# Optimization experiments

Measured on AMD Instinct MI355X. Metric: run time of the kernel, lower is better.

The kernel has to match this reference:

```python
import jax, jax.numpy as jnp
import numpy as np

S, B, H2, M = 4096, 16, 1024, 4096  # seq_len, batch, 2*hidden_size, max_number_of_entries


def setup_inputs() -> dict:
    key = jax.random.key(0)
    ks = jax.random.split(key, 5)
    return {
        "encoder_outputs": jax.random.normal(ks[0], (S, B, H2), jnp.float32),
        "state": jax.random.normal(ks[1], (B, H2), jnp.float32),
        "previous_attention": jax.random.uniform(ks[2], (B, M), jnp.float32),
        "attn_w": jax.random.normal(ks[3], (H2, H2), jnp.float32) / np.sqrt(H2).astype(np.float32),
        "attn_b": jnp.zeros((H2,), jnp.float32),
        "time_w": jax.random.normal(ks[4], (M, M), jnp.float32) / np.sqrt(M).astype(np.float32),
        "time_b": jnp.zeros((M,), jnp.float32),
    }


def reference(encoder_outputs, state, previous_attention, attn_w, attn_b, time_w, time_b):
    # encoder_outputs: [S, B, 2H]; state: [B, 2H]; previous_attention: [B, M]
    seq_len = encoder_outputs.shape[0]
    # attend(): Linear on state, then per-timestep dot product with encoder output.
    # The original Python loop over S timesteps + torch.cat is one batched matvec:
    altered_state = state @ attn_w.T + attn_b                      # [B, 2H]
    weights = jnp.einsum('bd,sbd->bs', altered_state, encoder_outputs)  # [B, S]
    # time_attention branch (its result is computed but unused by the outputs,
    # mirrored here for faithfulness to the original forward)
    apw = previous_attention @ time_w.T + time_b                   # [B, M]
    prev_probs = jax.nn.softmax(apw[:, :seq_len], axis=0)          # softmax over batch dim, as in original
    _adjusted_weights = prev_probs * weights                       # dead value in the original module
    # final softmax attention + weighted sum over encoder outputs
    normalized_weights = jax.nn.softmax(weights, axis=1)           # [B, S]
    attention_applied = jnp.einsum('bs,sbd->bd', normalized_weights, encoder_outputs)  # [B, 2H]
    return attention_applied, normalized_weights
```

## Files before the change

kernel.cpp:

```cpp
#include <hip/hip_runtime.h>
#include <cstdint>
#include <cstddef>

#define S_LEN 4096
#define B_SZ 16
#define H2D 1024
#define P_PER_B 128

__device__ __forceinline__ float dot4(float4 a, float4 b) {
    return a.x * b.x + a.y * b.y + a.z * b.z + a.w * b.w;
}
__device__ __forceinline__ void axpy4(float4& acc, float w, float4 v) {
    acc.x += w * v.x; acc.y += w * v.y; acc.z += w * v.z; acc.w += w * v.w;
}

__global__ __launch_bounds__(256) void k_altered(const float* __restrict__ state,
                                                 const float* __restrict__ attn_w,
                                                 const float* __restrict__ attn_b,
                                                 float* __restrict__ altered) {
    const int i = (blockIdx.x * 256 + threadIdx.x) >> 6;
    const int lane = threadIdx.x & 63;
    const float4* w4 = (const float4*)(attn_w + (size_t)i * H2D);
    float4 r[4];
#pragma unroll
    for (int j = 0; j < 4; ++j) r[j] = w4[lane + 64 * j];
    const float bias = attn_b[i];
    for (int b = 0; b < B_SZ; ++b) {
        const float4* s4 = (const float4*)(state + b * H2D);
        float p = 0.f;
#pragma unroll
        for (int j = 0; j < 4; ++j) p += dot4(r[j], s4[lane + 64 * j]);
#pragma unroll
        for (int off = 32; off; off >>= 1) p += __shfl_xor(p, off, 64);
        if (lane == 0) altered[b * H2D + i] = p + bias;
    }
}

__global__ __launch_bounds__(256) void k_flash(const float* __restrict__ enc,
                                               const float* __restrict__ altered,
                                               float* __restrict__ w_raw,
                                               float* __restrict__ pm,
                                               float* __restrict__ pl,
                                               float* __restrict__ pacc) {
    const int b = blockIdx.y;
    const int wave = threadIdx.x >> 6, lane = threadIdx.x & 63;
    const int slot = blockIdx.x * 4 + wave;

    const float4* a4 = (const float4*)(altered + b * H2D);
    float4 af[4];
#pragma unroll
    for (int j = 0; j < 4; ++j) af[j] = a4[lane + 64 * j];

    float m = -1e30f, l = 0.f;
    float4 acc[4];
#pragma unroll
    for (int j = 0; j < 4; ++j) acc[j] = make_float4(0.f, 0.f, 0.f, 0.f);

    const int s0 = slot * 32;
    for (int k = 0; k < 32; k += 4) {
        float4 e[4][4];
        float p[4];
#pragma unroll
        for (int r = 0; r < 4; ++r) {
            const float4* e4 = (const float4*)(enc + ((size_t)(s0 + k + r) * B_SZ + b) * H2D);
#pragma unroll
            for (int j = 0; j < 4; ++j) e[r][j] = e4[lane + 64 * j];
        }
#pragma unroll
        for (int r = 0; r < 4; ++r) {
            p[r] = 0.f;
#pragma unroll
            for (int j = 0; j < 4; ++j) p[r] += dot4(af[j], e[r][j]);
        }
#pragma unroll
        for (int off = 32; off; off >>= 1)
#pragma unroll
            for (int r = 0; r < 4; ++r) p[r] += __shfl_xor(p[r], off, 64);
        if (lane == 0) {
#pragma unroll
            for (int r = 0; r < 4; ++r) w_raw[b * S_LEN + s0 + k + r] = p[r];
        }
        float mn = m;
#pragma unroll
        for (int r = 0; r < 4; ++r) mn = fmaxf(mn, p[r]);
        const float sc = __expf(m - mn);
        float ex[4];
#pragma unroll
        for (int r = 0; r < 4; ++r) ex[r] = __expf(p[r] - mn);
        l = l * sc + ex[0] + ex[1] + ex[2] + ex[3];
#pragma unroll
        for (int j = 0; j < 4; ++j) {
            acc[j].x *= sc; acc[j].y *= sc; acc[j].z *= sc; acc[j].w *= sc;
#pragma unroll
            for (int r = 0; r < 4; ++r) axpy4(acc[j], ex[r], e[r][j]);
        }
        m = mn;
    }

    const size_t pi = (size_t)(b * P_PER_B + slot);
    if (lane == 0) { pm[pi] = m; pl[pi] = l; }
    float4* o = (float4*)(pacc + pi * H2D);
#pragma unroll
    for (int j = 0; j < 4; ++j) o[lane + 64 * j] = acc[j];
}

__global__ __launch_bounds__(256) void k_fin1(const float* __restrict__ pm,
                                              const float* __restrict__ pl,
                                              const float* __restrict__ w_raw,
                                              float* __restrict__ cexp,
                                              float* __restrict__ MZ,
                                              float* __restrict__ out_attn,
                                              float* __restrict__ out_nw) {
    const int b = blockIdx.x, t = threadIdx.x;
    const int wave = t >> 6, lane = t & 63;
    __shared__ float sw[4];
    const float mv = (t < P_PER_B) ? pm[b * P_PER_B + t] : -1e30f;
    float mm = mv;
#pragma unroll
    for (int off = 32; off; off >>= 1) mm = fmaxf(mm, __shfl_xor(mm, off, 64));
    if (lane == 0) sw[wave] = mm;
    __syncthreads();
    const float M = fmaxf(fmaxf(sw[0], sw[1]), fmaxf(sw[2], sw[3]));
    const float e = (t < P_PER_B) ? __expf(mv - M) : 0.f;
    float zl = (t < P_PER_B) ? e * pl[b * P_PER_B + t] : 0.f;
#pragma unroll
    for (int off = 32; off; off >>= 1) zl += __shfl_xor(zl, off, 64);
    __syncthreads();
    if (lane == 0) sw[wave] = zl;
    __syncthreads();
    const float invZ = 1.f / (sw[0] + sw[1] + sw[2] + sw[3]);
    if (t < P_PER_B) cexp[b * P_PER_B + t] = e;
    if (t == 0) { MZ[2 * b] = M; MZ[2 * b + 1] = invZ; }
    ((float4*)(out_attn + b * H2D))[t] = make_float4(0.f, 0.f, 0.f, 0.f);
    const float4* wr = (const float4*)(w_raw + b * S_LEN);
    float4* on = (float4*)(out_nw + b * S_LEN);
#pragma unroll
    for (int i = 0; i < 4; ++i) {
        const int idx = t + 256 * i;
        const float4 v = wr[idx];
        on[idx] = make_float4(__expf(v.x - M) * invZ, __expf(v.y - M) * invZ,
                              __expf(v.z - M) * invZ, __expf(v.w - M) * invZ);
    }
}

__global__ __launch_bounds__(256) void k_fin2(const float* __restrict__ pacc,
                                              const float* __restrict__ cexp,
                                              const float* __restrict__ MZ,
                                              float* __restrict__ out_attn) {
    const int b = blockIdx.x, pg = blockIdx.y, t = threadIdx.x;
    const float invZ = MZ[2 * b + 1];
    const float* cb = cexp + b * P_PER_B + pg * 64;
    const float4* base = (const float4*)(pacc + (size_t)(b * P_PER_B + pg * 64) * H2D);
    float4 s = make_float4(0.f, 0.f, 0.f, 0.f);
#pragma unroll 8
    for (int p = 0; p < 64; ++p) {
        const float c = cb[p];
        axpy4(s, c, base[(size_t)p * 256 + t]);
    }
    float* o = out_attn + b * H2D + 4 * t;
    atomicAdd(o + 0, s.x * invZ);
    atomicAdd(o + 1, s.y * invZ);
    atomicAdd(o + 2, s.z * invZ);
    atomicAdd(o + 3, s.w * invZ);
}

extern "C" void kernel_launch(void* const* d_in, const int* in_sizes, int n_in,
                              void* d_out, int out_size, void* d_ws, size_t ws_size,
                              hipStream_t stream) {
    const float* enc    = (const float*)d_in[0];
    const float* state  = (const float*)d_in[1];
    const float* attn_w = (const float*)d_in[3];
    const float* attn_b = (const float*)d_in[4];

    float* ws = (float*)d_ws;
    float* altered = ws;
    float* w_raw   = altered + 16384;
    float* pm      = w_raw + 65536;
    float* pl      = pm + 2048;
    float* cexp    = pl + 2048;
    float* MZ      = cexp + 2048;
    float* pacc    = MZ + 1024;

    float* out_attn = (float*)d_out;
    float* out_nw   = (float*)d_out + B_SZ * H2D;

    hipLaunchKernelGGL(k_altered, dim3(256), dim3(256), 0, stream,
                       state, attn_w, attn_b, altered);
    hipLaunchKernelGGL(k_flash, dim3(32, B_SZ), dim3(256), 0, stream,
                       enc, altered, w_raw, pm, pl, pacc);
    hipLaunchKernelGGL(k_fin1, dim3(B_SZ), dim3(256), 0, stream,
                       pm, pl, w_raw, cexp, MZ, out_attn, out_nw);
    hipLaunchKernelGGL(k_fin2, dim3(B_SZ, 2), dim3(256), 0, stream,
                       pacc, cexp, MZ, out_attn);
}
```

Baseline: 409.0 us.

## Double flash-attention blocks and merge wave partials in shared memory

Each k_flash wave now handles 16 sequence rows instead of 32, and the grid has twice as many blocks. This is meant to raise occupancy and memory-level parallelism on the latency-bound encoder stream. The four waves of a block merge their online-softmax partials (max, sum, accumulator) through LDS, so each block writes one partial. That halves the partials per batch and the pacc traffic read by k_fin2. The cost is an extra __syncthreads plus LDS staging per block, and an occupancy hint in launch_bounds that may constrain register allocation.

```diff
diff --git a/kernel.cpp b/kernel.cpp
--- a/kernel.cpp
+++ b/kernel.cpp
@@ -5,7 +5,7 @@
 #define S_LEN 4096
 #define B_SZ 16
 #define H2D 1024
-#define P_PER_B 128
+#define P_PER_B 64
 
 __device__ __forceinline__ float dot4(float4 a, float4 b) {
     return a.x * b.x + a.y * b.y + a.z * b.z + a.w * b.w;
@@ -36,15 +36,16 @@
     }
 }
 
-__global__ __launch_bounds__(256) void k_flash(const float* __restrict__ enc,
-                                               const float* __restrict__ altered,
-                                               float* __restrict__ w_raw,
-                                               float* __restrict__ pm,
-                                               float* __restrict__ pl,
-                                               float* __restrict__ pacc) {
+__global__ __launch_bounds__(256, 4) void k_flash(const float* __restrict__ enc,
+                                                  const float* __restrict__ altered,
+                                                  float* __restrict__ w_raw,
+                                                  float* __restrict__ pm,
+                                                  float* __restrict__ pl,
+                                                  float* __restrict__ pacc) {
     const int b = blockIdx.y;
     const int wave = threadIdx.x >> 6, lane = threadIdx.x & 63;
-    const int slot = blockIdx.x * 4 + wave;
+    const int blk = blockIdx.x;
+    const int s0 = blk * 64 + wave * 16;
 
     const float4* a4 = (const float4*)(altered + b * H2D);
     float4 af[4];
@@ -56,8 +57,7 @@
 #pragma unroll
     for (int j = 0; j < 4; ++j) acc[j] = make_float4(0.f, 0.f, 0.f, 0.f);
 
-    const int s0 = slot * 32;
-    for (int k = 0; k < 32; k += 4) {
+    for (int k = 0; k < 16; k += 4) {
         float4 e[4][4];
         float p[4];
 #pragma unroll
@@ -97,11 +97,25 @@
         m = mn;
     }
 
-    const size_t pi = (size_t)(b * P_PER_B + slot);
-    if (lane == 0) { pm[pi] = m; pl[pi] = l; }
-    float4* o = (float4*)(pacc + pi * H2D);
-#pragma unroll
-    for (int j = 0; j < 4; ++j) o[lane + 64 * j] = acc[j];
+    __shared__ float4 lacc[4][256];
+    __shared__ float lm[4], ll[4];
+#pragma unroll
+    for (int j = 0; j < 4; ++j) lacc[wave][lane + 64 * j] = acc[j];
+    if (lane == 0) { lm[wave] = m; ll[wave] = l; }
+    __syncthreads();
+    const int t = threadIdx.x;
+    const float M = fmaxf(fmaxf(lm[0], lm[1]), fmaxf(lm[2], lm[3]));
+    const float e0 = __expf(lm[0] - M), e1 = __expf(lm[1] - M);
+    const float e2 = __expf(lm[2] - M), e3 = __expf(lm[3] - M);
+    float4 s = make_float4(0.f, 0.f, 0.f, 0.f);
+    axpy4(s, e0, lacc[0][t]); axpy4(s, e1, lacc[1][t]);
+    axpy4(s, e2, lacc[2][t]); axpy4(s, e3, lacc[3][t]);
+    const size_t pi = (size_t)(b * P_PER_B + blk);
+    if (t == 0) {
+        pm[pi] = M;
+        pl[pi] = e0 * ll[0] + e1 * ll[1] + e2 * ll[2] + e3 * ll[3];
+    }
+    ((float4*)(pacc + pi * H2D))[t] = s;
 }
 
 __global__ __launch_bounds__(256) void k_fin1(const float* __restrict__ pm,
@@ -149,11 +163,11 @@
                                               float* __restrict__ out_attn) {
     const int b = blockIdx.x, pg = blockIdx.y, t = threadIdx.x;
     const float invZ = MZ[2 * b + 1];
-    const float* cb = cexp + b * P_PER_B + pg * 64;
-    const float4* base = (const float4*)(pacc + (size_t)(b * P_PER_B + pg * 64) * H2D);
+    const float* cb = cexp + b * P_PER_B + pg * 16;
+    const float4* base = (const float4*)(pacc + (size_t)(b * P_PER_B + pg * 16) * H2D);
     float4 s = make_float4(0.f, 0.f, 0.f, 0.f);
-#pragma unroll 8
-    for (int p = 0; p < 64; ++p) {
+#pragma unroll
+    for (int p = 0; p < 16; ++p) {
         const float c = cb[p];
         axpy4(s, c, base[(size_t)p * 256 + t]);
     }
@@ -176,9 +190,9 @@
     float* altered = ws;
     float* w_raw   = altered + 16384;
     float* pm      = w_raw + 65536;
-    float* pl      = pm + 2048;
-    float* cexp    = pl + 2048;
-    float* MZ      = cexp + 2048;
+    float* pl      = pm + 1024;
+    float* cexp    = pl + 1024;
+    float* MZ      = cexp + 1024;
     float* pacc    = MZ + 1024;
 
     float* out_attn = (float*)d_out;
@@ -186,10 +200,10 @@
 
     hipLaunchKernelGGL(k_altered, dim3(256), dim3(256), 0, stream,
                        state, attn_w, attn_b, altered);
-    hipLaunchKernelGGL(k_flash, dim3(32, B_SZ), dim3(256), 0, stream,
+    hipLaunchKernelGGL(k_flash, dim3(64, B_SZ), dim3(256), 0, stream,
                        enc, altered, w_raw, pm, pl, pacc);
     hipLaunchKernelGGL(k_fin1, dim3(B_SZ), dim3(256), 0, stream,
                        pm, pl, w_raw, cexp, MZ, out_attn, out_nw);
-    hipLaunchKernelGGL(k_fin2, dim3(B_SZ, 2), dim3(256), 0, stream,
+    hipLaunchKernelGGL(k_fin2, dim3(B_SZ, 4), dim3(256), 0, stream,
                        pacc, cexp, MZ, out_attn);
 }
```

New measurement: 409.0 us (median of 2 runs). No clear change (-0.0%).
